# Kernel tuning notes

Measured on AMD Instinct MI355X. Metric: run time of the kernel, lower is better.

## Reference

```python
import jax, jax.numpy as jnp
import numpy as np

N, D, K = 20000, 64, 32
EPS = 1e-5


def _knn_numpy(coords, k):
    # exact KNN, chunked; self is nearest (distance 0) -> index 0 column
    n = coords.shape[0]
    sq = (coords ** 2).sum(1)
    out = np.empty((n, k), np.int64)
    for s in range(0, n, 2000):
        c = coords[s:s + 2000]
        d = sq[None, :] - 2.0 * c @ coords.T  # row-constant term dropped
        part = np.argpartition(d, k - 1, axis=1)[:, :k]
        dp = np.take_along_axis(d, part, 1)
        order = np.argsort(dp, axis=1)
        out[s:s + 2000] = np.take_along_axis(part, order, 1)
    return out


def setup_inputs() -> dict:
    key = jax.random.key(0)
    ks = jax.random.split(key, 24)
    coords = jax.random.uniform(ks[0], (N, 3), dtype=jnp.float32) * 100.0
    feats = jax.random.normal(ks[1], (N, D), dtype=jnp.float32)
    knn_idx = jnp.asarray(_knn_numpy(np.asarray(coords), K + 1))  # [N, 33], self first

    def lin(k, fi, fo):
        return jax.random.normal(k, (fi, fo), dtype=jnp.float32) / np.sqrt(fi).astype(np.float32)

    def vec(k, fo):
        return jax.random.normal(k, (fo,), dtype=jnp.float32) * 0.01

    return {
        'coords': coords, 'feats': feats,
        'Wq': lin(ks[2], D, D), 'bq': vec(ks[3], D),
        'Wk': lin(ks[4], D, D), 'bk': vec(ks[5], D),
        'Wv': lin(ks[6], D, D), 'bv': vec(ks[7], D),
        'Wl1': lin(ks[8], 3, D), 'bl1': vec(ks[9], D),
        'Wl2': lin(ks[10], D, D), 'bl2': vec(ks[11], D),
        'Ww1': lin(ks[12], D, D), 'bw1': vec(ks[13], D),
        'Ww2': lin(ks[14], D, D), 'bw2': vec(ks[15], D),
        'g_att': jnp.ones((D,), jnp.float32), 'b_att': jnp.zeros((D,), jnp.float32),
        'Wsg': lin(ks[16], D + 3, D), 'bsg': vec(ks[17], D),
        'Wf': lin(ks[18], D, D), 'bf': vec(ks[19], D),
        'g_ff': jnp.ones((D,), jnp.float32), 'b_ff': jnp.zeros((D,), jnp.float32),
        'knn_idx': knn_idx,
    }


def _sparsemax_axis1(z):
    # sparsemax over axis=1 of [n, k, d] (matches torch Sparsemax(dim=1))
    zt = jnp.moveaxis(z, 1, -1)  # [n, d, k]
    z_sorted = jnp.flip(jnp.sort(zt, axis=-1), axis=-1)
    csum = jnp.cumsum(z_sorted, axis=-1)
    r = jnp.arange(1, zt.shape[-1] + 1, dtype=zt.dtype)
    support = 1.0 + r * z_sorted > csum
    k_sup = jnp.sum(support, axis=-1, keepdims=True)  # int, >=1
    tau = (jnp.take_along_axis(csum, k_sup - 1, axis=-1) - 1.0) / k_sup.astype(zt.dtype)
    return jnp.moveaxis(jnp.maximum(zt - tau, 0.0), -1, 1)


def _layernorm(x, g, b):
    m = jnp.mean(x, -1, keepdims=True)
    v = jnp.mean((x - m) ** 2, -1, keepdims=True)
    return g * (x - m) * jax.lax.rsqrt(v + EPS) + b


def reference(coords, feats, Wq, bq, Wk, bk, Wv, bv, Wl1, bl1, Wl2, bl2,
              Ww1, bw1, Ww2, bw2, g_att, b_att, Wsg, bsg, Wf, bf, g_ff, b_ff,
              knn_idx):
    n = feats.shape[0]
    # ---- RNSA (knn_points includes self: first K columns) ----
    idx = knn_idx[:, :K]                                   # [N, K]
    diff = coords[idx] - coords[:, None, :]                # [N, K, 3]
    fc = jax.nn.relu(diff @ Wl1 + bl1) @ Wl2 + bl2         # positional MLP [N, K, D]
    pe = fc + feats[idx]                                   # positional embedding
    Q = jax.nn.relu(feats @ Wq + bq)                       # [N, D]
    Kf = jax.nn.relu(pe @ Wk + bk)                         # [N, K, D]
    V = pe @ Wv + bv                                       # [N, K, D]
    rel = (Kf - Q[:, None, :]) * fc
    w = jax.nn.relu(rel @ Ww1 + bw1) @ Ww2 + bw2
    w = _sparsemax_axis1(w)                                # dropout: eval mode -> identity
    attn = jnp.einsum('nkd,nkd->nd', V, w)
    x_att = feats + attn                                   # RNSA residual (x + attended)
    x_att = x_att + feats                                  # outer residual in GraphFormer

    # ---- feed-forward: LayerNorm + SGConv(K=1) + linear + residual + LayerNorm ----
    h = _layernorm(x_att, g_att, b_att)
    x_in = jnp.concatenate([h, coords], axis=-1)           # [N, D+3]
    # knn_graph(loop=False): 32 nearest excluding self -> columns 1..32
    src = knn_idx[:, 1:K + 1].reshape(-1)
    dst = jnp.repeat(jnp.arange(n), K)
    self_idx = jnp.arange(n)
    src_all = jnp.concatenate([src, self_idx])             # gcn_norm adds self loops
    dst_all = jnp.concatenate([dst, self_idx])
    deg = jax.ops.segment_sum(jnp.ones_like(src_all, dtype=x_in.dtype), dst_all, num_segments=n)
    norm = jax.lax.rsqrt(deg[src_all] * deg[dst_all])
    agg = jax.ops.segment_sum(x_in[src_all] * norm[:, None], dst_all, num_segments=n)
    x_ff = agg @ Wsg + bsg
    x_ff = jax.nn.relu(x_ff)
    x_ff = x_ff @ Wf + bf                                  # dropout: eval -> identity
    x_out = x_ff + h
    return _layernorm(x_out, g_ff, b_ff)
```

## Files before the change

### kernel.cpp

```cpp
#include <hip/hip_runtime.h>

#define NPTS 20000
#define EPSF 1e-5f

typedef _Float16 half8 __attribute__((ext_vector_type(8)));
typedef float floatx4 __attribute__((ext_vector_type(4)));

__device__ __forceinline__ half8 ldWt(const _Float16* __restrict__ w,
                                      int c15, int g, int nt, int ks) {
  int c = nt * 16 + c15;
  int kg = ks * 4 + g;
  return *(const half8*)(w + c * 64 + ((kg ^ (c & 7)) << 3));
}

__device__ __forceinline__ half8 ldWtF32(const float* __restrict__ W,
                                         int c15, int g, int nt, int ks) {
  int c = nt * 16 + c15;
  half8 r;
#pragma unroll
  for (int j = 0; j < 8; ++j) r[j] = (_Float16)W[(ks * 32 + g * 8 + j) * 64 + c];
  return r;
}

__device__ __forceinline__ void stC(float* __restrict__ Tw, int c15, int g,
                                    int mt, int nt, floatx4 v) {
  int col = nt * 16 + c15;
  int chunk = mt * 4 + g;
  *(floatx4*)(Tw + col * 32 + ((chunk ^ (col & 7)) << 2)) = v;
}

__device__ __forceinline__ floatx4 ldCread(const float* __restrict__ Tw,
                                           int c15, int g, int mt, int nt) {
  int col = nt * 16 + c15;
  int chunk = mt * 4 + g;
  return *(const floatx4*)(Tw + col * 32 + ((chunk ^ (col & 7)) << 2));
}

__device__ __forceinline__ half8 ldA(const float* __restrict__ Tw,
                                     int c15, int g, int mt, int ks) {
  int m = mt * 16 + c15;
  half8 r;
#pragma unroll
  for (int j = 0; j < 8; ++j) {
    int c = ks * 32 + g * 8 + j;
    r[j] = (_Float16)Tw[c * 32 + (((m >> 2) ^ j) << 2) + (m & 3)];
  }
  return r;
}

__device__ __forceinline__ void ldAfrags(const float* __restrict__ Tw,
                                         int c15, int g, half8 a[2][2]) {
#pragma unroll
  for (int mt = 0; mt < 2; ++mt)
#pragma unroll
    for (int ks = 0; ks < 2; ++ks) a[mt][ks] = ldA(Tw, c15, g, mt, ks);
}

__device__ __forceinline__ void domm(const _Float16* __restrict__ w,
                                     const half8 a[2][2], int c15, int g,
                                     floatx4 acc[2][4]) {
#pragma unroll
  for (int ks = 0; ks < 2; ++ks)
#pragma unroll
    for (int nt = 0; nt < 4; ++nt) {
      half8 b = ldWt(w, c15, g, nt, ks);
#pragma unroll
      for (int mt = 0; mt < 2; ++mt)
        acc[mt][nt] = __builtin_amdgcn_mfma_f32_16x16x32_f16(a[mt][ks], b, acc[mt][nt], 0, 0, 0);
    }
}

__device__ __forceinline__ void domm1(const _Float16* __restrict__ w,
                                      const half8 a[2], int c15, int g,
                                      floatx4 acc[4]) {
#pragma unroll
  for (int ks = 0; ks < 2; ++ks)
#pragma unroll
    for (int nt = 0; nt < 4; ++nt) {
      half8 b = ldWt(w, c15, g, nt, ks);
      acc[nt] = __builtin_amdgcn_mfma_f32_16x16x32_f16(a[ks], b, acc[nt], 0, 0, 0);
    }
}

__global__ __launch_bounds__(256) void prep_q_kernel(
    const float* __restrict__ Wl2, const float* __restrict__ Wv,
    const float* __restrict__ Wk, const float* __restrict__ Ww1,
    const float* __restrict__ Ww2, const float* __restrict__ Wsg,
    const float* __restrict__ Wf, const float* __restrict__ Wq,
    const float* __restrict__ feats, const float* __restrict__ bq,
    _Float16* __restrict__ wtg, _Float16* __restrict__ Qh)
{
  if (blockIdx.x < 7) {
    const float* srcs[7] = {Wl2, Wv, Wk, Ww1, Ww2, Wsg, Wf};
    const float* src = srcs[blockIdx.x];
    _Float16* dst = wtg + blockIdx.x * 4096;
    int t = threadIdx.x;
#pragma unroll
    for (int i = 0; i < 16; ++i) {
      int lin = i * 256 + t;
      int k = lin >> 6, d = lin & 63;
      dst[d * 64 + (((k >> 3) ^ (d & 7)) << 3) + (k & 7)] = (_Float16)src[lin];
    }
    return;
  }
  const int wv = threadIdx.x >> 6, lane = threadIdx.x & 63;
  const int c15 = lane & 15, g = lane >> 4;
  const int n0 = ((blockIdx.x - 7) * 4 + wv) * 32;

  half8 a[2][2];
#pragma unroll
  for (int mt = 0; mt < 2; ++mt) {
    int r = n0 + mt * 16 + c15;
    if (r > NPTS - 1) r = NPTS - 1;
#pragma unroll
    for (int ks = 0; ks < 2; ++ks) {
      const float* p = feats + (size_t)r * 64 + ks * 32 + g * 8;
      float4 u0 = *(const float4*)p, u1 = *(const float4*)(p + 4);
      a[mt][ks][0] = (_Float16)u0.x; a[mt][ks][1] = (_Float16)u0.y;
      a[mt][ks][2] = (_Float16)u0.z; a[mt][ks][3] = (_Float16)u0.w;
      a[mt][ks][4] = (_Float16)u1.x; a[mt][ks][5] = (_Float16)u1.y;
      a[mt][ks][6] = (_Float16)u1.z; a[mt][ks][7] = (_Float16)u1.w;
    }
  }
  floatx4 acc[2][4] = {};
#pragma unroll
  for (int ks = 0; ks < 2; ++ks)
#pragma unroll
    for (int nt = 0; nt < 4; ++nt) {
      half8 b = ldWtF32(Wq, c15, g, nt, ks);
#pragma unroll
      for (int mt = 0; mt < 2; ++mt)
        acc[mt][nt] = __builtin_amdgcn_mfma_f32_16x16x32_f16(a[mt][ks], b, acc[mt][nt], 0, 0, 0);
    }
#pragma unroll
  for (int nt = 0; nt < 4; ++nt) {
    float bqv = bq[nt * 16 + c15];
#pragma unroll
    for (int mt = 0; mt < 2; ++mt)
#pragma unroll
      for (int r = 0; r < 4; ++r) {
        int n = n0 + mt * 16 + g * 4 + r;
        if (n < NPTS)
          Qh[(size_t)n * 64 + nt * 16 + c15] = (_Float16)fmaxf(acc[mt][nt][r] + bqv, 0.f);
      }
  }
}

__global__ __launch_bounds__(256, 4) void attn_kernel(
    const float* __restrict__ coords, const float* __restrict__ feats,
    const float* __restrict__ bk, const float* __restrict__ bv,
    const float* __restrict__ Wl1, const float* __restrict__ bl1,
    const float* __restrict__ bl2, const float* __restrict__ bw1,
    const float* __restrict__ bw2, const float* __restrict__ g_att,
    const float* __restrict__ b_att, const int* __restrict__ knn,
    const _Float16* __restrict__ wtg, const _Float16* __restrict__ Qh,
    _Float16* __restrict__ h_out)
{
  __shared__ float Tsh[4][2048];
  const int wv = threadIdx.x >> 6, lane = threadIdx.x & 63;
  const int c15 = lane & 15, g = lane >> 4;
  const int n = blockIdx.x * 4 + wv;
  float* Tw = Tsh[wv];
  const int* row = knn + (size_t)n * 33;

  const _Float16* wt_l2 = wtg;
  const _Float16* wt_v  = wtg + 4096;
  const _Float16* wt_k  = wtg + 8192;
  const _Float16* wt_w1 = wtg + 12288;
  const _Float16* wt_w2 = wtg + 16384;

  half8 aH[2][2];
  {
    float cnx = coords[(size_t)n * 3], cny = coords[(size_t)n * 3 + 1],
          cnz = coords[(size_t)n * 3 + 2];
#pragma unroll
    for (int ks = 0; ks < 2; ++ks) {
      int c0 = ks * 32 + g * 8;
      float4 wx0 = *(const float4*)(Wl1 + c0),       wx1 = *(const float4*)(Wl1 + c0 + 4);
      float4 wy0 = *(const float4*)(Wl1 + 64 + c0),  wy1 = *(const float4*)(Wl1 + 64 + c0 + 4);
      float4 wz0 = *(const float4*)(Wl1 + 128 + c0), wz1 = *(const float4*)(Wl1 + 128 + c0 + 4);
      float4 bb0 = *(const float4*)(bl1 + c0),       bb1 = *(const float4*)(bl1 + c0 + 4);
      float wx[8] = {wx0.x,wx0.y,wx0.z,wx0.w,wx1.x,wx1.y,wx1.z,wx1.w};
      float wy[8] = {wy0.x,wy0.y,wy0.z,wy0.w,wy1.x,wy1.y,wy1.z,wy1.w};
      float wz[8] = {wz0.x,wz0.y,wz0.z,wz0.w,wz1.x,wz1.y,wz1.z,wz1.w};
      float bb[8] = {bb0.x,bb0.y,bb0.z,bb0.w,bb1.x,bb1.y,bb1.z,bb1.w};
#pragma unroll
      for (int mt = 0; mt < 2; ++mt) {
        int id = row[mt * 16 + c15];
        float dx = coords[(size_t)id * 3] - cnx;
        float dy = coords[(size_t)id * 3 + 1] - cny;
        float dz = coords[(size_t)id * 3 + 2] - cnz;
#pragma unroll
        for (int j = 0; j < 8; ++j)
          aH[mt][ks][j] = (_Float16)fmaxf(dx * wx[j] + dy * wy[j] + dz * wz[j] + bb[j], 0.f);
      }
    }
  }

  {
    floatx4 fcacc[2][4] = {};
    domm(wt_l2, aH, c15, g, fcacc);
#pragma unroll
    for (int nt = 0; nt < 4; ++nt) {
      float b = bl2[nt * 16 + c15];
#pragma unroll
      for (int mt = 0; mt < 2; ++mt) stC(Tw, c15, g, mt, nt, fcacc[mt][nt] + b);
    }
  }
  __builtin_amdgcn_wave_barrier();

  half8 aP[2][2];
#pragma unroll
  for (int mt = 0; mt < 2; ++mt) {
    int m = mt * 16 + c15;
    int rn = row[m];
#pragma unroll
    for (int ks = 0; ks < 2; ++ks) {
      const float* fp = feats + (size_t)rn * 64 + ks * 32 + g * 8;
      float4 u0 = *(const float4*)fp, u1 = *(const float4*)(fp + 4);
      float fv[8] = {u0.x,u0.y,u0.z,u0.w,u1.x,u1.y,u1.z,u1.w};
#pragma unroll
      for (int j = 0; j < 8; ++j) {
        int c = ks * 32 + g * 8 + j;
        float fcv = Tw[c * 32 + (((m >> 2) ^ j) << 2) + (m & 3)];
        aP[mt][ks][j] = (_Float16)(fcv + fv[j]);
      }
    }
  }
  __builtin_amdgcn_wave_barrier();

  {
    floatx4 KR[2][4] = {};
    domm(wt_k, aP, c15, g, KR);
    __builtin_amdgcn_wave_barrier();
#pragma unroll
    for (int nt = 0; nt < 4; ++nt) {
      float bkv = bk[nt * 16 + c15];
      float q4 = (float)Qh[(size_t)n * 64 + nt * 16 + c15];
#pragma unroll
      for (int mt = 0; mt < 2; ++mt) {
        floatx4 fcq = ldCread(Tw, c15, g, mt, nt);
        floatx4 v;
#pragma unroll
        for (int r = 0; r < 4; ++r)
          v[r] = (fmaxf(KR[mt][nt][r] + bkv, 0.f) - q4) * fcq[r];
        stC(Tw, c15, g, mt, nt, v);
      }
    }
  }
  __builtin_amdgcn_wave_barrier();
  half8 aR[2][2];
  ldAfrags(Tw, c15, g, aR);

  {
    floatx4 W1[2][4] = {};
    domm(wt_w1, aR, c15, g, W1);
    __builtin_amdgcn_wave_barrier();
#pragma unroll
    for (int nt = 0; nt < 4; ++nt) {
      float b = bw1[nt * 16 + c15];
#pragma unroll
      for (int mt = 0; mt < 2; ++mt) {
        floatx4 v;
#pragma unroll
        for (int r = 0; r < 4; ++r) v[r] = fmaxf(W1[mt][nt][r] + b, 0.f);
        stC(Tw, c15, g, mt, nt, v);
      }
    }
  }
  __builtin_amdgcn_wave_barrier();
  half8 aW[2][2];
  ldAfrags(Tw, c15, g, aW);

  {
    floatx4 WW[2][4] = {};
    domm(wt_w2, aW, c15, g, WW);
    __builtin_amdgcn_wave_barrier();
#pragma unroll
    for (int nt = 0; nt < 4; ++nt) {
      float b = bw2[nt * 16 + c15];
#pragma unroll
      for (int mt = 0; mt < 2; ++mt) stC(Tw, c15, g, mt, nt, WW[mt][nt] + b);
    }
  }
  __builtin_amdgcn_wave_barrier();

  float tau;
  {
    float a[32];
#pragma unroll
    for (int i = 0; i < 8; ++i) {
      floatx4 ch = *(const floatx4*)(Tw + lane * 32 + ((i ^ (lane & 7)) << 2));
#pragma unroll
      for (int r = 0; r < 4; ++r) a[i * 4 + r] = ch[r];
    }
#pragma unroll
    for (int size = 2; size <= 32; size <<= 1) {
#pragma unroll
      for (int stride = size >> 1; stride > 0; stride >>= 1) {
#pragma unroll
        for (int i = 0; i < 32; ++i) {
          int j = i ^ stride;
          if (j > i) {
            float x = a[i], y = a[j];
            float lo = fminf(x, y), hi = fmaxf(x, y);
            bool up = ((i & size) == 0);
            a[i] = up ? hi : lo;
            a[j] = up ? lo : hi;
          }
        }
      }
    }
    float csum = 0.f, csel = 0.f;
    int ksup = 1;
#pragma unroll
    for (int i = 0; i < 32; ++i) {
      csum += a[i];
      if (1.0f + (float)(i + 1) * a[i] > csum) { ksup = i + 1; csel = csum; }
    }
    tau = (csel - 1.0f) / (float)ksup;
  }

  floatx4 V[2][4] = {};
  domm(wt_v, aP, c15, g, V);
#pragma unroll
  for (int nt = 0; nt < 4; ++nt) {
    float b = bv[nt * 16 + c15];
#pragma unroll
    for (int mt = 0; mt < 2; ++mt) V[mt][nt] += b;
  }

  float x4[4];
#pragma unroll
  for (int nt = 0; nt < 4; ++nt) {
    float t4 = __shfl(tau, nt * 16 + c15, 64);
    float ssum = 0.f;
#pragma unroll
    for (int mt = 0; mt < 2; ++mt) {
      floatx4 w4 = ldCread(Tw, c15, g, mt, nt);
#pragma unroll
      for (int r = 0; r < 4; ++r)
        ssum += fmaxf(w4[r] - t4, 0.f) * V[mt][nt][r];
    }
    ssum += __shfl_xor(ssum, 16, 64);
    ssum += __shfl_xor(ssum, 32, 64);
    x4[nt] = 2.f * feats[(size_t)n * 64 + nt * 16 + c15] + ssum;
  }

  float sum = x4[0] + x4[1] + x4[2] + x4[3];
  float sum2 = x4[0] * x4[0] + x4[1] * x4[1] + x4[2] * x4[2] + x4[3] * x4[3];
#pragma unroll
  for (int m = 1; m < 16; m <<= 1) {
    sum += __shfl_xor(sum, m, 64);
    sum2 += __shfl_xor(sum2, m, 64);
  }
  float mean = sum * (1.f / 64.f);
  float var = sum2 * (1.f / 64.f) - mean * mean;
  float inv = rsqrtf(var + EPSF);
  h_out[(size_t)n * 64 + lane] =
      (_Float16)(g_att[lane] * (x4[g] - mean) * inv + b_att[lane]);
}

__global__ __launch_bounds__(256) void gconv_kernel(
    const float* __restrict__ coords, const _Float16* __restrict__ h,
    const _Float16* __restrict__ wtg, const float* __restrict__ Wsg,
    const float* __restrict__ bsg, const float* __restrict__ bf,
    const float* __restrict__ g_ff, const float* __restrict__ b_ff,
    const int* __restrict__ knn, float* __restrict__ out)
{
  __shared__ float agg_s[16 * 68];
  __shared__ float cm_s[16 * 4];
  __shared__ float T2[2048];
  const int wv = __builtin_amdgcn_readfirstlane(threadIdx.x >> 6);
  const int lane = threadIdx.x & 63;
  const int c15 = lane & 15, g = lane >> 4;
  const int n0 = blockIdx.x * 16;
  const float inv33 = 1.0f / 33.0f;
  const _Float16* wt_sg = wtg + 5 * 4096;
  const _Float16* wt_f  = wtg + 6 * 4096;

#pragma unroll
  for (int i = 0; i < 4; ++i) {
    int pl = wv * 4 + i;
    int p = n0 + pl;
    const int* row = knn + (size_t)p * 33;
    float acc = (float)h[(size_t)p * 64 + lane];
#pragma unroll 8
    for (int k = 1; k <= 32; ++k) {
      int idx = __builtin_amdgcn_readfirstlane(row[k]);
      acc += (float)h[(size_t)idx * 64 + lane];
    }
    agg_s[pl * 68 + lane] = acc * inv33;

    float sx = 0.f, sy = 0.f, sz = 0.f;
    if (lane < 33) {
      int src = (lane == 0) ? p : row[lane];
      sx = coords[(size_t)src * 3];
      sy = coords[(size_t)src * 3 + 1];
      sz = coords[(size_t)src * 3 + 2];
    }
#pragma unroll
    for (int m = 1; m < 64; m <<= 1) {
      sx += __shfl_xor(sx, m, 64);
      sy += __shfl_xor(sy, m, 64);
      sz += __shfl_xor(sz, m, 64);
    }
    if (lane == 0) {
      cm_s[pl * 4 + 0] = sx * inv33;
      cm_s[pl * 4 + 1] = sy * inv33;
      cm_s[pl * 4 + 2] = sz * inv33;
    }
  }
  __syncthreads();
  if (wv != 0) return;

  half8 aA[2];
#pragma unroll
  for (int ks = 0; ks < 2; ++ks) {
    const float* pr = agg_s + c15 * 68 + ks * 32 + g * 8;
    float4 u0 = *(const float4*)pr, u1 = *(const float4*)(pr + 4);
    aA[ks][0] = (_Float16)u0.x; aA[ks][1] = (_Float16)u0.y;
    aA[ks][2] = (_Float16)u0.z; aA[ks][3] = (_Float16)u0.w;
    aA[ks][4] = (_Float16)u1.x; aA[ks][5] = (_Float16)u1.y;
    aA[ks][6] = (_Float16)u1.z; aA[ks][7] = (_Float16)u1.w;
  }

  float cmx[4], cmy[4], cmz[4];
#pragma unroll
  for (int r = 0; r < 4; ++r) {
    int pl = g * 4 + r;
    cmx[r] = cm_s[pl * 4 + 0];
    cmy[r] = cm_s[pl * 4 + 1];
    cmz[r] = cm_s[pl * 4 + 2];
  }

  {
    floatx4 C1[4] = {};
    domm1(wt_sg, aA, c15, g, C1);
#pragma unroll
    for (int nt = 0; nt < 4; ++nt) {
      int col = nt * 16 + c15;
      float b = bsg[col];
      float w64 = Wsg[4096 + col], w65 = Wsg[4160 + col], w66 = Wsg[4224 + col];
      floatx4 v;
#pragma unroll
      for (int r = 0; r < 4; ++r)
        v[r] = fmaxf(C1[nt][r] + b + cmx[r] * w64 + cmy[r] * w65 + cmz[r] * w66, 0.f);
      stC(T2, c15, g, 0, nt, v);
    }
  }
  __builtin_amdgcn_wave_barrier();
  half8 aT[2];
  aT[0] = ldA(T2, c15, g, 0, 0);
  aT[1] = ldA(T2, c15, g, 0, 1);

  floatx4 C2[4] = {};
  domm1(wt_f, aT, c15, g, C2);
#pragma unroll
  for (int nt = 0; nt < 4; ++nt) {
    int col = nt * 16 + c15;
    float b = bf[col];
#pragma unroll
    for (int r = 0; r < 4; ++r)
      C2[nt][r] += b + (float)h[(size_t)(n0 + g * 4 + r) * 64 + col];
  }
#pragma unroll
  for (int r = 0; r < 4; ++r) {
    float s = C2[0][r] + C2[1][r] + C2[2][r] + C2[3][r];
    float s2 = C2[0][r] * C2[0][r] + C2[1][r] * C2[1][r] +
               C2[2][r] * C2[2][r] + C2[3][r] * C2[3][r];
#pragma unroll
    for (int m = 1; m < 16; m <<= 1) {
      s += __shfl_xor(s, m, 64);
      s2 += __shfl_xor(s2, m, 64);
    }
    float mean = s * (1.f / 64.f);
    float var = s2 * (1.f / 64.f) - mean * mean;
    float inv = rsqrtf(var + EPSF);
    int prow = n0 + g * 4 + r;
#pragma unroll
    for (int nt = 0; nt < 4; ++nt) {
      int col = nt * 16 + c15;
      out[(size_t)prow * 64 + col] =
          g_ff[col] * (C2[nt][r] - mean) * inv + b_ff[col];
    }
  }
}

extern "C" void kernel_launch(void* const* d_in, const int* in_sizes, int n_in,
                              void* d_out, int out_size, void* d_ws, size_t ws_size,
                              hipStream_t stream) {
  (void)in_sizes; (void)n_in; (void)out_size; (void)ws_size;
  const float* coords = (const float*)d_in[0];
  const float* feats  = (const float*)d_in[1];
  const float* Wq  = (const float*)d_in[2];  const float* bq  = (const float*)d_in[3];
  const float* Wk  = (const float*)d_in[4];  const float* bk  = (const float*)d_in[5];
  const float* Wv  = (const float*)d_in[6];  const float* bv  = (const float*)d_in[7];
  const float* Wl1 = (const float*)d_in[8];  const float* bl1 = (const float*)d_in[9];
  const float* Wl2 = (const float*)d_in[10]; const float* bl2 = (const float*)d_in[11];
  const float* Ww1 = (const float*)d_in[12]; const float* bw1 = (const float*)d_in[13];
  const float* Ww2 = (const float*)d_in[14]; const float* bw2 = (const float*)d_in[15];
  const float* g_att = (const float*)d_in[16]; const float* b_att = (const float*)d_in[17];
  const float* Wsg = (const float*)d_in[18]; const float* bsg = (const float*)d_in[19];
  const float* Wf  = (const float*)d_in[20]; const float* bf  = (const float*)d_in[21];
  const float* g_ff = (const float*)d_in[22]; const float* b_ff = (const float*)d_in[23];
  const int* knn = (const int*)d_in[24];

  _Float16* h   = (_Float16*)d_ws;
  _Float16* wtg = (_Float16*)((char*)d_ws + 2621440);
  _Float16* Qh  = (_Float16*)((char*)d_ws + 2621440 + 57344);
  float* out = (float*)d_out;

  prep_q_kernel<<<dim3(164), dim3(256), 0, stream>>>(
      Wl2, Wv, Wk, Ww1, Ww2, Wsg, Wf, Wq, feats, bq, wtg, Qh);
  attn_kernel<<<dim3(NPTS / 4), dim3(256), 0, stream>>>(
      coords, feats, bk, bv, Wl1, bl1, bl2, bw1, bw2,
      g_att, b_att, knn, wtg, Qh, h);
  gconv_kernel<<<dim3(NPTS / 16), dim3(256), 0, stream>>>(
      coords, h, wtg, Wsg, bsg, bf, g_ff, b_ff, knn, out);
}
```

Before: 212.1 us.

## Fuse Q projection into attention kernel and shrink prep to weight conversion

The query projection (feats @ Wq + bq, relu) moves out of the prep kernel and into the attention kernel. Each wave computes its own point's Q row with one MFMA pass over a 16-row tile, using the pre-swizzled fp16 Wq. The prep kernel now only converts the eight weight matrices. This removes the fp16 Q buffer round trip through global memory and most of the prep kernel's work. The cost is a redundant 16-row MFMA per wave, where only one row is used, plus extra register pressure in the attention kernel.

```diff
diff --git a/kernel.cpp b/kernel.cpp
--- a/kernel.cpp
+++ b/kernel.cpp
@@ -13,15 +13,6 @@
   return *(const half8*)(w + c * 64 + ((kg ^ (c & 7)) << 3));
 }
 
-__device__ __forceinline__ half8 ldWtF32(const float* __restrict__ W,
-                                         int c15, int g, int nt, int ks) {
-  int c = nt * 16 + c15;
-  half8 r;
-#pragma unroll
-  for (int j = 0; j < 8; ++j) r[j] = (_Float16)W[(ks * 32 + g * 8 + j) * 64 + c];
-  return r;
-}
-
 __device__ __forceinline__ void stC(float* __restrict__ Tw, int c15, int g,
                                     int mt, int nt, floatx4 v) {
   int col = nt * 16 + c15;
@@ -82,79 +73,34 @@
     }
 }
 
-__global__ __launch_bounds__(256) void prep_q_kernel(
+__global__ __launch_bounds__(256) void prep_kernel(
     const float* __restrict__ Wl2, const float* __restrict__ Wv,
     const float* __restrict__ Wk, const float* __restrict__ Ww1,
     const float* __restrict__ Ww2, const float* __restrict__ Wsg,
     const float* __restrict__ Wf, const float* __restrict__ Wq,
-    const float* __restrict__ feats, const float* __restrict__ bq,
-    _Float16* __restrict__ wtg, _Float16* __restrict__ Qh)
+    _Float16* __restrict__ wtg)
 {
-  if (blockIdx.x < 7) {
-    const float* srcs[7] = {Wl2, Wv, Wk, Ww1, Ww2, Wsg, Wf};
-    const float* src = srcs[blockIdx.x];
-    _Float16* dst = wtg + blockIdx.x * 4096;
-    int t = threadIdx.x;
-#pragma unroll
-    for (int i = 0; i < 16; ++i) {
-      int lin = i * 256 + t;
-      int k = lin >> 6, d = lin & 63;
-      dst[d * 64 + (((k >> 3) ^ (d & 7)) << 3) + (k & 7)] = (_Float16)src[lin];
-    }
-    return;
-  }
-  const int wv = threadIdx.x >> 6, lane = threadIdx.x & 63;
-  const int c15 = lane & 15, g = lane >> 4;
-  const int n0 = ((blockIdx.x - 7) * 4 + wv) * 32;
-
-  half8 a[2][2];
-#pragma unroll
-  for (int mt = 0; mt < 2; ++mt) {
-    int r = n0 + mt * 16 + c15;
-    if (r > NPTS - 1) r = NPTS - 1;
-#pragma unroll
-    for (int ks = 0; ks < 2; ++ks) {
-      const float* p = feats + (size_t)r * 64 + ks * 32 + g * 8;
-      float4 u0 = *(const float4*)p, u1 = *(const float4*)(p + 4);
-      a[mt][ks][0] = (_Float16)u0.x; a[mt][ks][1] = (_Float16)u0.y;
-      a[mt][ks][2] = (_Float16)u0.z; a[mt][ks][3] = (_Float16)u0.w;
-      a[mt][ks][4] = (_Float16)u1.x; a[mt][ks][5] = (_Float16)u1.y;
-      a[mt][ks][6] = (_Float16)u1.z; a[mt][ks][7] = (_Float16)u1.w;
-    }
-  }
-  floatx4 acc[2][4] = {};
-#pragma unroll
-  for (int ks = 0; ks < 2; ++ks)
-#pragma unroll
-    for (int nt = 0; nt < 4; ++nt) {
-      half8 b = ldWtF32(Wq, c15, g, nt, ks);
-#pragma unroll
-      for (int mt = 0; mt < 2; ++mt)
-        acc[mt][nt] = __builtin_amdgcn_mfma_f32_16x16x32_f16(a[mt][ks], b, acc[mt][nt], 0, 0, 0);
-    }
-#pragma unroll
-  for (int nt = 0; nt < 4; ++nt) {
-    float bqv = bq[nt * 16 + c15];
-#pragma unroll
-    for (int mt = 0; mt < 2; ++mt)
-#pragma unroll
-      for (int r = 0; r < 4; ++r) {
-        int n = n0 + mt * 16 + g * 4 + r;
-        if (n < NPTS)
-          Qh[(size_t)n * 64 + nt * 16 + c15] = (_Float16)fmaxf(acc[mt][nt][r] + bqv, 0.f);
-      }
+  const float* srcs[8] = {Wl2, Wv, Wk, Ww1, Ww2, Wsg, Wf, Wq};
+  const float* src = srcs[blockIdx.x];
+  _Float16* dst = wtg + blockIdx.x * 4096;
+  int t = threadIdx.x;
+#pragma unroll
+  for (int i = 0; i < 16; ++i) {
+    int lin = i * 256 + t;
+    int k = lin >> 6, d = lin & 63;
+    dst[d * 64 + (((k >> 3) ^ (d & 7)) << 3) + (k & 7)] = (_Float16)src[lin];
   }
 }
 
 __global__ __launch_bounds__(256, 4) void attn_kernel(
     const float* __restrict__ coords, const float* __restrict__ feats,
-    const float* __restrict__ bk, const float* __restrict__ bv,
+    const float* __restrict__ bq, const float* __restrict__ bk,
+    const float* __restrict__ bv,
     const float* __restrict__ Wl1, const float* __restrict__ bl1,
     const float* __restrict__ bl2, const float* __restrict__ bw1,
     const float* __restrict__ bw2, const float* __restrict__ g_att,
     const float* __restrict__ b_att, const int* __restrict__ knn,
-    const _Float16* __restrict__ wtg, const _Float16* __restrict__ Qh,
-    _Float16* __restrict__ h_out)
+    const _Float16* __restrict__ wtg, _Float16* __restrict__ h_out)
 {
   __shared__ float Tsh[4][2048];
   const int wv = threadIdx.x >> 6, lane = threadIdx.x & 63;
@@ -168,6 +114,26 @@
   const _Float16* wt_k  = wtg + 8192;
   const _Float16* wt_w1 = wtg + 12288;
   const _Float16* wt_w2 = wtg + 16384;
+  const _Float16* wt_q  = wtg + 7 * 4096;
+
+  float q4[4];
+  {
+    half8 aF[2];
+#pragma unroll
+    for (int ks = 0; ks < 2; ++ks) {
+      const float* fp = feats + (size_t)n * 64 + ks * 32 + g * 8;
+      float4 u0 = *(const float4*)fp, u1 = *(const float4*)(fp + 4);
+      aF[ks][0] = (_Float16)u0.x; aF[ks][1] = (_Float16)u0.y;
+      aF[ks][2] = (_Float16)u0.z; aF[ks][3] = (_Float16)u0.w;
+      aF[ks][4] = (_Float16)u1.x; aF[ks][5] = (_Float16)u1.y;
+      aF[ks][6] = (_Float16)u1.z; aF[ks][7] = (_Float16)u1.w;
+    }
+    floatx4 CQ[4] = {};
+    domm1(wt_q, aF, c15, g, CQ);
+#pragma unroll
+    for (int nt = 0; nt < 4; ++nt)
+      q4[nt] = fmaxf(CQ[nt][0] + bq[nt * 16 + c15], 0.f);
+  }
 
   half8 aH[2][2];
   {
@@ -236,14 +202,13 @@
 #pragma unroll
     for (int nt = 0; nt < 4; ++nt) {
       float bkv = bk[nt * 16 + c15];
-      float q4 = (float)Qh[(size_t)n * 64 + nt * 16 + c15];
 #pragma unroll
       for (int mt = 0; mt < 2; ++mt) {
         floatx4 fcq = ldCread(Tw, c15, g, mt, nt);
         floatx4 v;
 #pragma unroll
         for (int r = 0; r < 4; ++r)
-          v[r] = (fmaxf(KR[mt][nt][r] + bkv, 0.f) - q4) * fcq[r];
+          v[r] = (fmaxf(KR[mt][nt][r] + bkv, 0.f) - q4[nt]) * fcq[r];
         stC(Tw, c15, g, mt, nt, v);
       }
     }
@@ -508,14 +473,13 @@
 
   _Float16* h   = (_Float16*)d_ws;
   _Float16* wtg = (_Float16*)((char*)d_ws + 2621440);
-  _Float16* Qh  = (_Float16*)((char*)d_ws + 2621440 + 57344);
   float* out = (float*)d_out;
 
-  prep_q_kernel<<<dim3(164), dim3(256), 0, stream>>>(
-      Wl2, Wv, Wk, Ww1, Ww2, Wsg, Wf, Wq, feats, bq, wtg, Qh);
+  prep_kernel<<<dim3(8), dim3(256), 0, stream>>>(
+      Wl2, Wv, Wk, Ww1, Ww2, Wsg, Wf, Wq, wtg);
   attn_kernel<<<dim3(NPTS / 4), dim3(256), 0, stream>>>(
-      coords, feats, bk, bv, Wl1, bl1, bl2, bw1, bw2,
-      g_att, b_att, knn, wtg, Qh, h);
+      coords, feats, bq, bk, bv, Wl1, bl1, bl2, bw1, bw2,
+      g_att, b_att, knn, wtg, h);
   gconv_kernel<<<dim3(NPTS / 16), dim3(256), 0, stream>>>(
       coords, h, wtg, Wsg, bsg, bf, g_ff, b_ff, knn, out);
 }
```

New measurement: 212.5 us. About the same (+0.2%).
